# Kernel optimization log

Measured on AMD Instinct MI355X. Metric: run time of the kernel, lower is better.

The kernel has to match this reference:

```python
import jax, jax.numpy as jnp
import numpy as np

N_POINTS = 2_000_000
N_VOXELS = 200_000
RESOLUTION = 0.05

# Corner bit pattern matching child_id encoding in find_voxel_indices:
# corner k has bits (k&1, (k>>1)&1, (k>>2)&1) along (x, y, z).
_BITS = np.stack([[(k >> 0) & 1, (k >> 1) & 1, (k >> 2) & 1] for k in range(8)]).astype(np.float32)  # [8,3]


def setup_inputs() -> dict:
    key = jax.random.key(0)
    ks = jax.random.split(key, 7)
    points = jax.random.uniform(ks[0], (N_POINTS, 3), dtype=jnp.float32) * 10.0
    voxel_indices = jax.random.randint(ks[1], (N_POINTS,), 0, N_VOXELS)
    voxel_centers = jax.random.uniform(ks[2], (N_VOXELS, 3), dtype=jnp.float32) * 10.0
    vertex_indices = jax.random.randint(ks[3], (N_VOXELS, 8), 0, N_VOXELS).astype(jnp.int32)
    # discrete voxel sizes (structure[:, -1]); leaves at varying depths -> sizes in {1,2,4}
    voxel_sizes = (2 ** jax.random.randint(ks[4], (N_VOXELS,), 0, 3)).astype(jnp.int32)
    sdf_priors = jax.random.normal(ks[5], (N_VOXELS,), dtype=jnp.float32) * 0.1
    grad_priors = jax.random.normal(ks[6], (N_VOXELS, 3), dtype=jnp.float32) * 0.1
    return {
        "points": points,
        "voxel_indices": voxel_indices,
        "voxel_centers": voxel_centers,
        "vertex_indices": vertex_indices,
        "voxel_sizes": voxel_sizes,
        "sdf_priors": sdf_priors,
        "grad_priors": grad_priors,
    }


def reference(points, voxel_indices, voxel_centers, vertex_indices, voxel_sizes,
              sdf_priors, grad_priors):
    bits = jnp.asarray(_BITS)                              # [8,3]
    vc = voxel_centers[voxel_indices]                      # [P,3] gather
    vi = vertex_indices[voxel_indices].astype(jnp.int32)   # [P,8]
    size = voxel_sizes[voxel_indices].astype(points.dtype)[:, None] * RESOLUTION  # [P,1]

    # local trilinear coordinates in [0,1] within the voxel
    t = (points - vc) / size + 0.5                         # [P,3]
    # trilinear weights per corner
    w = jnp.prod(jnp.where(bits[None] > 0, t[:, None, :], 1.0 - t[:, None, :]), axis=-1)  # [P,8]

    vals = sdf_priors[vi]                                  # [P,8]
    grads = grad_priors[vi]                                # [P,8,3]
    corner = vc[:, None, :] + (bits[None] - 0.5) * size[:, None, :]  # [P,8,3]
    delta = points[:, None, :] - corner                    # [P,8,3]

    # gradient-augmented trilinear: first-order Taylor from each corner, trilinearly blended
    sdf = jnp.sum(w * (vals + jnp.sum(grads * delta, axis=-1)), axis=-1)  # [P]
    return sdf, voxel_indices
```

## Files before the change

kernel.cpp:

```cpp
#include <hip/hip_runtime.h>
#include <hip/hip_fp16.h>

#define RESOLUTION 0.05f

__device__ __forceinline__ unsigned int pack_h2(float a, float b) {
    __half2 h = __floats2half2_rn(a, b);
    union { __half2 h2; unsigned int ui; } cv; cv.h2 = h;
    return cv.ui;
}
__device__ __forceinline__ float2 unpack_h2(unsigned int u) {
    union { unsigned int ui; __half2 h2; } cv; cv.ui = u;
    return __half22float2(cv.h2);
}

__global__ __launch_bounds__(256) void pack_kernel(
    const float* __restrict__ voxel_centers,
    const int*   __restrict__ voxel_sizes,
    const float* __restrict__ sdf_priors,
    const float* __restrict__ grad_priors,
    const int*   __restrict__ vertex_indices,
    float4* __restrict__ vmeta,
    uint4*  __restrict__ corners,
    int V)
{
    int v = blockIdx.x * blockDim.x + threadIdx.x;
    if (v >= V) return;

    float size = (float)voxel_sizes[v] * RESOLUTION;

    float4 m;
    m.x = voxel_centers[3*v + 0];
    m.y = voxel_centers[3*v + 1];
    m.z = voxel_centers[3*v + 2];
    m.w = size;
    vmeta[v] = m;

    const int4* vi4 = (const int4*)(vertex_indices + 8*v);
    int4 va = vi4[0];
    int4 vb = vi4[1];
    int vid[8] = {va.x, va.y, va.z, va.w, vb.x, vb.y, vb.z, vb.w};

    unsigned int words[16];
    #pragma unroll
    for (int k = 0; k < 8; ++k) {
        int u = vid[k];
        float s  = sdf_priors[u];
        float Bx = size * grad_priors[3*u + 0];
        float By = size * grad_priors[3*u + 1];
        float Bz = size * grad_priors[3*u + 2];
        float bx = (float)( k       & 1);
        float by = (float)((k >> 1) & 1);
        float bz = (float)((k >> 2) & 1);
        float A  = s - (Bx*bx + By*by + Bz*bz);
        words[2*k + 0] = pack_h2(A,  Bx);
        words[2*k + 1] = pack_h2(By, Bz);
    }

    uint4* out = corners + 4*v;
    #pragma unroll
    for (int q = 0; q < 4; ++q)
        out[q] = make_uint4(words[4*q+0], words[4*q+1], words[4*q+2], words[4*q+3]);
}

__global__ __launch_bounds__(256) void octree_sdf_h16_kernel(
    const float*  __restrict__ points,
    const int*    __restrict__ voxel_indices,
    const float4* __restrict__ vmeta,
    const uint4*  __restrict__ corners,
    float* __restrict__ out_sdf,
    float* __restrict__ out_idx,
    int n)
{
    int i = blockIdx.x * blockDim.x + threadIdx.x;
    if (i >= n) return;

    float px = points[3*i + 0];
    float py = points[3*i + 1];
    float pz = points[3*i + 2];

    int v = voxel_indices[i];

    float4 m = vmeta[v];

    const uint4* cr = corners + 4*v;
    uint4 q0 = cr[0], q1 = cr[1], q2 = cr[2], q3 = cr[3];
    unsigned int w_[16] = {q0.x,q0.y,q0.z,q0.w, q1.x,q1.y,q1.z,q1.w,
                           q2.x,q2.y,q2.z,q2.w, q3.x,q3.y,q3.z,q3.w};

    float tx = (px - m.x) / m.w + 0.5f;
    float ty = (py - m.y) / m.w + 0.5f;
    float tz = (pz - m.z) / m.w + 0.5f;
    float ux = 1.0f - tx, uy = 1.0f - ty, uz = 1.0f - tz;

    float wt[8] = { ux*uy*uz, tx*uy*uz, ux*ty*uz, tx*ty*uz,
                    ux*uy*tz, tx*uy*tz, ux*ty*tz, tx*ty*tz };

    float sdf = 0.0f;
    #pragma unroll
    for (int k = 0; k < 8; ++k) {
        float2 ab = unpack_h2(w_[2*k + 0]);
        float2 cd = unpack_h2(w_[2*k + 1]);
        sdf += wt[k] * (ab.x + ab.y*tx + cd.x*ty + cd.y*tz);
    }

    out_sdf[i] = sdf;
    out_idx[i] = (float)v;
}

__global__ __launch_bounds__(256) void octree_sdf_direct_kernel(
    const float* __restrict__ points,
    const int*   __restrict__ voxel_indices,
    const float* __restrict__ voxel_centers,
    const int*   __restrict__ vertex_indices,
    const int*   __restrict__ voxel_sizes,
    const float* __restrict__ sdf_priors,
    const float* __restrict__ grad_priors,
    float* __restrict__ out_sdf,
    float* __restrict__ out_idx,
    int n)
{
    int i = blockIdx.x * blockDim.x + threadIdx.x;
    if (i >= n) return;

    float px = points[3*i + 0];
    float py = points[3*i + 1];
    float pz = points[3*i + 2];

    int v = voxel_indices[i];

    float cx = voxel_centers[3*v + 0];
    float cy = voxel_centers[3*v + 1];
    float cz = voxel_centers[3*v + 2];
    float size = (float)voxel_sizes[v] * RESOLUTION;

    float tx = (px - cx) / size + 0.5f;
    float ty = (py - cy) / size + 0.5f;
    float tz = (pz - cz) / size + 0.5f;

    const int4* vi4 = (const int4*)(vertex_indices + 8*v);
    int4 va = vi4[0];
    int4 vb = vi4[1];
    int vid[8] = {va.x, va.y, va.z, va.w, vb.x, vb.y, vb.z, vb.w};

    float half_size = 0.5f * size;
    float sdf = 0.0f;

    #pragma unroll
    for (int k = 0; k < 8; ++k) {
        float bx = (float)( k       & 1);
        float by = (float)((k >> 1) & 1);
        float bz = (float)((k >> 2) & 1);

        float w = (bx > 0.0f ? tx : 1.0f - tx)
                * (by > 0.0f ? ty : 1.0f - ty)
                * (bz > 0.0f ? tz : 1.0f - tz);

        int u = vid[k];
        float val = sdf_priors[u];
        float gx  = grad_priors[3*u + 0];
        float gy  = grad_priors[3*u + 1];
        float gz  = grad_priors[3*u + 2];

        float dx = px - (cx + (2.0f*bx - 1.0f) * half_size);
        float dy = py - (cy + (2.0f*by - 1.0f) * half_size);
        float dz = pz - (cz + (2.0f*bz - 1.0f) * half_size);

        sdf += w * (val + gx*dx + gy*dy + gz*dz);
    }

    out_sdf[i] = sdf;
    out_idx[i] = (float)v;
}

extern "C" void kernel_launch(void* const* d_in, const int* in_sizes, int n_in,
                              void* d_out, int out_size, void* d_ws, size_t ws_size,
                              hipStream_t stream) {
    const float* points         = (const float*)d_in[0];
    const int*   voxel_indices  = (const int*)  d_in[1];
    const float* voxel_centers  = (const float*)d_in[2];
    const int*   vertex_indices = (const int*)  d_in[3];
    const int*   voxel_sizes    = (const int*)  d_in[4];
    const float* sdf_priors     = (const float*)d_in[5];
    const float* grad_priors    = (const float*)d_in[6];

    int n = in_sizes[1];
    int V = in_sizes[4];
    float* out_sdf = (float*)d_out;
    float* out_idx = out_sdf + n;

    int block = 256;
    int gridV = (V + block - 1) / block;
    int gridP = (n + block - 1) / block;

    size_t need = (size_t)V * (16 + 64);

    if (ws_size >= need) {
        float4* vmeta   = (float4*)d_ws;
        uint4*  corners = (uint4*)(vmeta + V);
        size_t off = ((size_t)V * 16 + 63) & ~(size_t)63;
        corners = (uint4*)((char*)d_ws + off);

        pack_kernel<<<gridV, block, 0, stream>>>(
            voxel_centers, voxel_sizes, sdf_priors, grad_priors, vertex_indices,
            vmeta, corners, V);

        octree_sdf_h16_kernel<<<gridP, block, 0, stream>>>(
            points, voxel_indices, vmeta, corners, out_sdf, out_idx, n);
    } else {
        octree_sdf_direct_kernel<<<gridP, block, 0, stream>>>(
            points, voxel_indices, voxel_centers, vertex_indices,
            voxel_sizes, sdf_priors, grad_priors, out_sdf, out_idx, n);
    }
}
```

Before: 159.3 us.

## Precompute per-voxel polynomial coefficients and pack metadata into one 64-byte record

The pack kernel now expands the gradient-augmented trilinear blend into 20 per-voxel polynomial coefficients in t, stored as fp16. The voxel center and size are stored in fp32 in the same 64-byte record, so each point does a single 64B gather instead of separate 16B and 64B gathers. The per-point kernel evaluates the polynomial directly and multiplies by a reciprocal instead of dividing. The main aim is to cut gathered bytes and per-point arithmetic. The risk is that storing the expanded coefficients in fp16 may lose more precision than storing per-corner values.

```diff
diff --git a/kernel.cpp b/kernel.cpp
--- a/kernel.cpp
+++ b/kernel.cpp
@@ -13,34 +13,37 @@
     return __half22float2(cv.h2);
 }
 
-__global__ __launch_bounds__(256) void pack_kernel(
+
+__global__ __launch_bounds__(256) void pack_rec_kernel(
     const float* __restrict__ voxel_centers,
     const int*   __restrict__ voxel_sizes,
     const float* __restrict__ sdf_priors,
     const float* __restrict__ grad_priors,
     const int*   __restrict__ vertex_indices,
-    float4* __restrict__ vmeta,
-    uint4*  __restrict__ corners,
+    uint4*       __restrict__ rec,
     int V)
 {
     int v = blockIdx.x * blockDim.x + threadIdx.x;
     if (v >= V) return;
 
     float size = (float)voxel_sizes[v] * RESOLUTION;
-
-    float4 m;
-    m.x = voxel_centers[3*v + 0];
-    m.y = voxel_centers[3*v + 1];
-    m.z = voxel_centers[3*v + 2];
-    m.w = size;
-    vmeta[v] = m;
+    float cx = voxel_centers[3*v + 0];
+    float cy = voxel_centers[3*v + 1];
+    float cz = voxel_centers[3*v + 2];
 
     const int4* vi4 = (const int4*)(vertex_indices + 8*v);
     int4 va = vi4[0];
     int4 vb = vi4[1];
     int vid[8] = {va.x, va.y, va.z, va.w, vb.x, vb.y, vb.z, vb.w};
 
-    unsigned int words[16];
+    float c[3][3][3];
+    #pragma unroll
+    for (int i = 0; i < 3; ++i)
+        #pragma unroll
+        for (int j = 0; j < 3; ++j)
+            #pragma unroll
+            for (int l = 0; l < 3; ++l) c[i][j][l] = 0.0f;
+
     #pragma unroll
     for (int k = 0; k < 8; ++k) {
         int u = vid[k];
@@ -48,25 +51,59 @@
         float Bx = size * grad_priors[3*u + 0];
         float By = size * grad_priors[3*u + 1];
         float Bz = size * grad_priors[3*u + 2];
-        float bx = (float)( k       & 1);
-        float by = (float)((k >> 1) & 1);
-        float bz = (float)((k >> 2) & 1);
-        float A  = s - (Bx*bx + By*by + Bz*bz);
-        words[2*k + 0] = pack_h2(A,  Bx);
-        words[2*k + 1] = pack_h2(By, Bz);
+        int bx = k & 1, by = (k >> 1) & 1, bz = (k >> 2) & 1;
+        float A = s - (Bx*(float)bx + By*(float)by + Bz*(float)bz);
+
+        float wx[2] = { bx ? 0.0f : 1.0f, bx ? 1.0f : -1.0f };
+        float wy[2] = { by ? 0.0f : 1.0f, by ? 1.0f : -1.0f };
+        float wz[2] = { bz ? 0.0f : 1.0f, bz ? 1.0f : -1.0f };
+
+        #pragma unroll
+        for (int i = 0; i < 2; ++i)
+            #pragma unroll
+            for (int j = 0; j < 2; ++j)
+                #pragma unroll
+                for (int l = 0; l < 2; ++l) {
+                    float wc = wx[i] * wy[j] * wz[l];
+                    c[i][j][l]     += wc * A;
+                    c[i+1][j][l]   += wc * Bx;
+                    c[i][j+1][l]   += wc * By;
+                    c[i][j][l+1]   += wc * Bz;
+                }
     }
 
-    uint4* out = corners + 4*v;
-    #pragma unroll
-    for (int q = 0; q < 4; ++q)
-        out[q] = make_uint4(words[4*q+0], words[4*q+1], words[4*q+2], words[4*q+3]);
-}
-
-__global__ __launch_bounds__(256) void octree_sdf_h16_kernel(
-    const float*  __restrict__ points,
-    const int*    __restrict__ voxel_indices,
-    const float4* __restrict__ vmeta,
-    const uint4*  __restrict__ corners,
+    float cf[20];
+    #pragma unroll
+    for (int l = 0; l < 2; ++l)
+        #pragma unroll
+        for (int j = 0; j < 2; ++j)
+            #pragma unroll
+            for (int i = 0; i < 2; ++i) cf[i + 2*j + 4*l] = c[i][j][l];
+    #pragma unroll
+    for (int l = 0; l < 2; ++l)
+        #pragma unroll
+        for (int j = 0; j < 2; ++j) {
+            cf[8  + j + 2*l] = c[2][j][l];
+            cf[12 + j + 2*l] = c[j][2][l];
+            cf[16 + j + 2*l] = c[j][l][2];
+        }
+
+    union { float f; unsigned int u; } fx, fy, fz, fs;
+    fx.f = cx; fy.f = cy; fz.f = cz; fs.f = size;
+
+    uint4* out = rec + 4*v;
+    out[0] = make_uint4(fx.u, fy.u, fz.u, fs.u);
+    out[1] = make_uint4(pack_h2(cf[0],cf[1]),  pack_h2(cf[2],cf[3]),
+                        pack_h2(cf[4],cf[5]),  pack_h2(cf[6],cf[7]));
+    out[2] = make_uint4(pack_h2(cf[8],cf[9]),  pack_h2(cf[10],cf[11]),
+                        pack_h2(cf[12],cf[13]),pack_h2(cf[14],cf[15]));
+    out[3] = make_uint4(pack_h2(cf[16],cf[17]),pack_h2(cf[18],cf[19]), 0u, 0u);
+}
+
+__global__ __launch_bounds__(256) void octree_sdf_poly_kernel(
+    const float* __restrict__ points,
+    const int*   __restrict__ voxel_indices,
+    const uint4* __restrict__ rec,
     float* __restrict__ out_sdf,
     float* __restrict__ out_idx,
     int n)
@@ -80,30 +117,44 @@
 
     int v = voxel_indices[i];
 
-    float4 m = vmeta[v];
-
-    const uint4* cr = corners + 4*v;
-    uint4 q0 = cr[0], q1 = cr[1], q2 = cr[2], q3 = cr[3];
-    unsigned int w_[16] = {q0.x,q0.y,q0.z,q0.w, q1.x,q1.y,q1.z,q1.w,
-                           q2.x,q2.y,q2.z,q2.w, q3.x,q3.y,q3.z,q3.w};
-
-    float tx = (px - m.x) / m.w + 0.5f;
-    float ty = (py - m.y) / m.w + 0.5f;
-    float tz = (pz - m.z) / m.w + 0.5f;
-    float ux = 1.0f - tx, uy = 1.0f - ty, uz = 1.0f - tz;
-
-    float wt[8] = { ux*uy*uz, tx*uy*uz, ux*ty*uz, tx*ty*uz,
-                    ux*uy*tz, tx*uy*tz, ux*ty*tz, tx*ty*tz };
-
-    float sdf = 0.0f;
-    #pragma unroll
-    for (int k = 0; k < 8; ++k) {
-        float2 ab = unpack_h2(w_[2*k + 0]);
-        float2 cd = unpack_h2(w_[2*k + 1]);
-        sdf += wt[k] * (ab.x + ab.y*tx + cd.x*ty + cd.y*tz);
-    }
-
-    out_sdf[i] = sdf;
+    const uint4* r = rec + 4*v;
+    uint4 q0 = r[0], q1 = r[1], q2 = r[2], q3 = r[3];
+
+    union { unsigned int u; float f; } m0, m1, m2, m3;
+    m0.u = q0.x; m1.u = q0.y; m2.u = q0.z; m3.u = q0.w;
+    float inv = 1.0f / m3.f;
+
+    float tx = (px - m0.f) * inv + 0.5f;
+    float ty = (py - m1.f) * inv + 0.5f;
+    float tz = (pz - m2.f) * inv + 0.5f;
+
+    float2 p01 = unpack_h2(q1.x), p23 = unpack_h2(q1.y);
+    float2 p45 = unpack_h2(q1.z), p67 = unpack_h2(q1.w);
+    float2 p89 = unpack_h2(q2.x), pab = unpack_h2(q2.y);
+    float2 pcd = unpack_h2(q2.z), pef = unpack_h2(q2.w);
+    float2 pgh = unpack_h2(q3.x), pij = unpack_h2(q3.y);
+
+    float txty = tx * ty;
+    float txtz = tx * tz;
+    float tytz = ty * tz;
+    float txtytz = txty * tz;
+
+    float s = p01.x
+            + p01.y * tx
+            + p23.x * ty
+            + p23.y * txty
+            + p45.x * tz
+            + p45.y * txtz
+            + p67.x * tytz
+            + p67.y * txtytz;
+    float tx2 = tx * tx;
+    s += tx2 * (p89.x + p89.y * ty + pab.x * tz + pab.y * tytz);
+    float ty2 = ty * ty;
+    s += ty2 * (pcd.x + pcd.y * tx + pef.x * tz + pef.y * txtz);
+    float tz2 = tz * tz;
+    s += tz2 * (pgh.x + pgh.y * tx + pij.x * ty + pij.y * txty);
+
+    out_sdf[i] = s;
     out_idx[i] = (float)v;
 }
 
@@ -192,20 +243,17 @@
     int gridV = (V + block - 1) / block;
     int gridP = (n + block - 1) / block;
 
-    size_t need = (size_t)V * (16 + 64);
+    size_t need = (size_t)V * 64;
 
     if (ws_size >= need) {
-        float4* vmeta   = (float4*)d_ws;
-        uint4*  corners = (uint4*)(vmeta + V);
-        size_t off = ((size_t)V * 16 + 63) & ~(size_t)63;
-        corners = (uint4*)((char*)d_ws + off);
-
-        pack_kernel<<<gridV, block, 0, stream>>>(
+        uint4* rec = (uint4*)d_ws;
+
+        pack_rec_kernel<<<gridV, block, 0, stream>>>(
             voxel_centers, voxel_sizes, sdf_priors, grad_priors, vertex_indices,
-            vmeta, corners, V);
-
-        octree_sdf_h16_kernel<<<gridP, block, 0, stream>>>(
-            points, voxel_indices, vmeta, corners, out_sdf, out_idx, n);
+            rec, V);
+
+        octree_sdf_poly_kernel<<<gridP, block, 0, stream>>>(
+            points, voxel_indices, rec, out_sdf, out_idx, n);
     } else {
         octree_sdf_direct_kernel<<<gridP, block, 0, stream>>>(
             points, voxel_indices, voxel_centers, vertex_indices,
```

Result: faster. 141.5 us (-11.2%).
